# Kernel optimization log

Hardware: AMD Instinct MI355X
Metric: run time of the kernel (lower is better)

## Reference

```python
import jax, jax.numpy as jnp
from jax import lax
import numpy as np

B, T, F = 256, 256, 40
H, A, HORIZON = 256, 64, 60
D_SP = 192


def setup_inputs() -> dict:
    key = jax.random.key(0)
    ks = jax.random.split(key, 16)
    s = 0.05  # weight scale to keep activations stable
    return {
        'x': jax.random.normal(ks[0], (B, T, F), jnp.float32),
        'W_sp': jax.random.normal(ks[1], (F, D_SP), jnp.float32) * s,
        'b_sp': jnp.zeros((D_SP,), jnp.float32),
        'Wx_ef': jax.random.normal(ks[2], (D_SP, 4 * H), jnp.float32) * s,
        'Wh_ef': jax.random.normal(ks[3], (H, 4 * H), jnp.float32) * s,
        'b_ef': jnp.zeros((4 * H,), jnp.float32),
        'Wx_eb': jax.random.normal(ks[4], (D_SP, 4 * H), jnp.float32) * s,
        'Wh_eb': jax.random.normal(ks[5], (H, 4 * H), jnp.float32) * s,
        'b_eb': jnp.zeros((4 * H,), jnp.float32),
        'We': jax.random.normal(ks[6], (2 * H, A), jnp.float32) * s,
        'Wd': jax.random.normal(ks[7], (H, A), jnp.float32) * s,
        'v': jax.random.normal(ks[8], (A,), jnp.float32) * s,
        'Wx_d': jax.random.normal(ks[9], (1 + 2 * H, 4 * H), jnp.float32) * s,
        'Wh_d': jax.random.normal(ks[10], (H, 4 * H), jnp.float32) * s,
        'b_d': jnp.zeros((4 * H,), jnp.float32),
        'W_ih': jax.random.normal(ks[11], (2 * H, H), jnp.float32) * s,
        'b_ih': jnp.zeros((H,), jnp.float32),
        'W_ic': jax.random.normal(ks[12], (2 * H, H), jnp.float32) * s,
        'b_ic': jnp.zeros((H,), jnp.float32),
        'Wo': jax.random.normal(ks[13], (H, 1), jnp.float32) * s,
        'bo': jnp.zeros((1,), jnp.float32),
    }


def _lstm_cell(x_t, h, c, Wx, Wh, b):
    g = x_t @ Wx + h @ Wh + b
    i, f, gg, o = jnp.split(g, 4, axis=-1)  # torch gate order i,f,g,o
    c = jax.nn.sigmoid(f) * c + jax.nn.sigmoid(i) * jnp.tanh(gg)
    h = jax.nn.sigmoid(o) * jnp.tanh(c)
    return h, c


def _lstm_scan(xs_tbd, Wx, Wh, b):
    # xs_tbd: [T, B, D] -> hs [T, B, H]
    h0 = jnp.zeros((xs_tbd.shape[1], Wh.shape[0]), xs_tbd.dtype)
    c0 = jnp.zeros_like(h0)
    def step(carry, x_t):
        h, c = carry
        h, c = _lstm_cell(x_t, h, c, Wx, Wh, b)
        return (h, c), h
    _, hs = lax.scan(step, (h0, c0), xs_tbd)
    return hs


def reference(x, W_sp, b_sp, Wx_ef, Wh_ef, b_ef, Wx_eb, Wh_eb, b_eb,
              We, Wd, v, Wx_d, Wh_d, b_d, W_ih, b_ih, W_ic, b_ic, Wo, bo):
    # spatial encoder (stand-in for DeepLOBEncoder): [B,T,F] -> [B,T,192]
    h_spatial = x @ W_sp + b_sp
    xs = jnp.swapaxes(h_spatial, 0, 1)          # [T, B, 192]
    hs_f = _lstm_scan(xs, Wx_ef, Wh_ef, b_ef)    # [T, B, H]
    hs_b = _lstm_scan(xs[::-1], Wx_eb, Wh_eb, b_eb)[::-1]
    enc_out = jnp.swapaxes(jnp.concatenate([hs_f, hs_b], axis=-1), 0, 1)  # [B,T,2H]

    enc_mean = enc_out.mean(axis=1)
    dec_h = jnp.tanh(enc_mean @ W_ih + b_ih)     # [B, H]
    dec_c = jnp.tanh(enc_mean @ W_ic + b_ic)

    enc_proj = enc_out @ We                      # [B, T, A] precomputed (same math)
    prev_y = ((x[:, -1, 0] + x[:, -1, 2]) / 2.0)[:, None]  # ask_idx=0, bid_idx=2

    def dec_step(carry, _):
        h, c, py = carry
        e = jnp.tanh(enc_proj + (h @ Wd)[:, None, :])        # [B,T,A]
        scores = e @ v                                        # [B,T]
        w = jax.nn.softmax(scores, axis=1)
        context = jnp.einsum('bt,bth->bh', w, enc_out)        # [B,2H]
        dec_in = jnp.concatenate([py, context], axis=1)       # [B,1+2H]
        h, c = _lstm_cell(dec_in, h, c, Wx_d, Wh_d, b_d)
        y = h @ Wo + bo                                       # [B,1]
        return (h, c, lax.stop_gradient(y)), y[:, 0]

    _, ys = lax.scan(dec_step, (dec_h, dec_c, prev_y), None, length=HORIZON)
    return jnp.swapaxes(ys, 0, 1)  # [B, horizon]
```

## Files before the change

kernel.cpp:

```cpp
#include <hip/hip_runtime.h>
#include <cmath>

#define B_ 256
#define T_ 256
#define F_ 40
#define H_ 256
#define A_ 64
#define HOR_ 60
#define DSP_ 192
#define ENC_NBLK 128
#define GRP_SZ 16
#define WSTR 456

typedef unsigned short u16;
typedef unsigned int u32;
typedef __attribute__((ext_vector_type(8))) short bf16x8;
typedef __attribute__((ext_vector_type(4))) float f32x4;
typedef __attribute__((ext_vector_type(8))) u32 u32x8;
typedef __attribute__((ext_vector_type(4))) u32 u32x4;

__device__ __forceinline__ float sigm(float x){ return 1.f/(1.f+expf(-x)); }

__device__ __forceinline__ u16 f2bf(float x){
  u32 u = __float_as_uint(x);
  u32 r = (u + 0x7FFFu + ((u>>16)&1u)) >> 16;
  return (u16)r;
}
__device__ __forceinline__ float bf2f(u16 h){ return __uint_as_float(((u32)h)<<16); }
__device__ __forceinline__ u32 packsplit(float x){
  u16 hi = f2bf(x);
  u16 lo = f2bf(x - bf2f(hi));
  return (u32)hi | ((u32)lo<<16);
}
__device__ __forceinline__ float unpack2f(u32 v){
  return __uint_as_float(v<<16) + __uint_as_float(v & 0xFFFF0000u);
}

__device__ __forceinline__ float wred_sum(float v){
  #pragma unroll
  for (int o=32;o>0;o>>=1) v += __shfl_xor(v,o);
  return v;
}
__device__ __forceinline__ float wred_max(float v){
  #pragma unroll
  for (int o=32;o>0;o>>=1) v = fmaxf(v,__shfl_xor(v,o));
  return v;
}

__global__ void conv_w(const float* __restrict__ Wx, const float* __restrict__ Wh,
                       u16* __restrict__ hi, u16* __restrict__ lo,
                       int KX, int Ktot, int N){
  int idx = blockIdx.x*256 + threadIdx.x;
  if (idx >= N*Ktot) return;
  int n = idx / Ktot, k = idx - n*Ktot;
  float w = (k < KX) ? Wx[(size_t)k*N + n] : Wh[(size_t)(k-KX)*N + n];
  u16 h = f2bf(w);
  hi[idx] = h;
  lo[idx] = f2bf(w - bf2f(h));
}

__global__ __launch_bounds__(192) void spatial_proj(
    const float* __restrict__ x, const float* __restrict__ W, const float* __restrict__ bsp,
    u32* __restrict__ hsp32){
  __shared__ float Ws[40][192];
  __shared__ float xr[40];
  int t = blockIdx.x, tid = threadIdx.x;
  for (int i = tid; i < 40*192; i += 192){ int k = i/192, c = i-k*192; Ws[k][c] = W[i]; }
  float bb = bsp[tid];
  __syncthreads();
  for (int b=0; b<B_; b++){
    if (tid < 40) xr[tid] = x[((size_t)b*T_ + t)*F_ + tid];
    __syncthreads();
    float acc = bb;
    #pragma unroll
    for (int k=0;k<40;k++) acc += xr[k]*Ws[k][tid];
    hsp32[((size_t)t*B_ + b)*DSP_ + tid] = packsplit(acc);
    __syncthreads();
  }
}

__global__ __launch_bounds__(256) void enc_scan(
    const u32* __restrict__ hsp32,
    const u16* __restrict__ W_hi, const u16* __restrict__ W_lo,
    const float* __restrict__ b_ef, const float* __restrict__ b_eb,
    u32* __restrict__ hbuf, u32* __restrict__ eo32, int* __restrict__ bar)
{
  extern __shared__ u16 smem[];
  u16* Whi = smem;
  u16* Wlo = smem + 4*16*WSTR;
  const int bid = blockIdx.x;
  const int grp = bid & 7;
  const int nt  = bid >> 3;
  const int dir = grp >> 2;
  const int m0  = (grp & 3) * 64;
  const int u0  = nt * 16;
  const int tid = threadIdx.x;
  const int wave = tid >> 6, lane = tid & 63;
  const int lrow = lane & 15, kblk = lane >> 4;
  const int koff = kblk * 8;
  {
    const size_t wbase = ((size_t)dir*1024 + u0) * 448;
    for (int idx = tid; idx < 4*16*448; idx += 256){
      int g = idx / (16*448);
      int r = idx - g*(16*448);
      int j = r / 448;
      int k = r - j*448;
      size_t go = wbase + ((size_t)g*256 + j)*448 + k;
      Whi[(g*16 + j)*WSTR + k] = W_hi[go];
      Wlo[(g*16 + j)*WSTR + k] = W_lo[go];
    }
  }
  const float* bias = dir ? b_eb : b_ef;
  float bg4[4];
  #pragma unroll
  for (int g=0; g<4; g++) bg4[g] = bias[g*H_ + u0 + lrow];
  __syncthreads();

  const int mrow = m0 + wave*16;
  const int arow = mrow + lrow;
  u32* hP0 = hbuf + (size_t)dir*(B_*H_);
  u32* hP1 = hbuf + (size_t)(2+dir)*(B_*H_);
  int* gbar = bar + grp*T_;
  float c_reg[4] = {0.f,0.f,0.f,0.f};

  for (int s=0; s<T_; s++){
    const int t = dir ? (T_-1-s) : s;
    f32x4 acc[4] = {};
    const u32* abase = hsp32 + ((size_t)t*B_ + arow)*DSP_;
    #pragma unroll
    for (int ks=0; ks<6; ks++){
      int kb = ks*32 + koff;
      u32x8 la = *(const u32x8*)(abase + kb);
      bf16x8 ah, al;
      #pragma unroll
      for (int j=0;j<8;j++){ ah[j]=(short)(la[j]&0xFFFFu); al[j]=(short)(la[j]>>16); }
      #pragma unroll
      for (int g=0; g<4; g++){
        bf16x8 bh = *(const bf16x8*)(Whi + (g*16+lrow)*WSTR + kb);
        bf16x8 bl = *(const bf16x8*)(Wlo + (g*16+lrow)*WSTR + kb);
        acc[g] = __builtin_amdgcn_mfma_f32_16x16x32_bf16(ah, bh, acc[g], 0,0,0);
        acc[g] = __builtin_amdgcn_mfma_f32_16x16x32_bf16(ah, bl, acc[g], 0,0,0);
        acc[g] = __builtin_amdgcn_mfma_f32_16x16x32_bf16(al, bh, acc[g], 0,0,0);
      }
    }
    if (s > 0){
      if (tid == 0){
        while (__hip_atomic_load(&gbar[s-1], __ATOMIC_ACQUIRE, __HIP_MEMORY_SCOPE_AGENT) < GRP_SZ)
          __builtin_amdgcn_s_sleep(1);
      }
      __syncthreads();
    }
    const u32* hin = (s & 1) ? hP1 : hP0;
    u32* hout      = (s & 1) ? hP0 : hP1;
    const u32* hbase = hin + (size_t)arow*H_;
    #pragma unroll
    for (int ks=0; ks<8; ks++){
      int kb = ks*32 + koff;
      u32x8 la = *(const u32x8*)(hbase + kb);
      bf16x8 ah, al;
      #pragma unroll
      for (int j=0;j<8;j++){ ah[j]=(short)(la[j]&0xFFFFu); al[j]=(short)(la[j]>>16); }
      #pragma unroll
      for (int g=0; g<4; g++){
        bf16x8 bh = *(const bf16x8*)(Whi + (g*16+lrow)*WSTR + 192 + kb);
        bf16x8 bl = *(const bf16x8*)(Wlo + (g*16+lrow)*WSTR + 192 + kb);
        acc[g] = __builtin_amdgcn_mfma_f32_16x16x32_bf16(ah, bh, acc[g], 0,0,0);
        acc[g] = __builtin_amdgcn_mfma_f32_16x16x32_bf16(ah, bl, acc[g], 0,0,0);
        acc[g] = __builtin_amdgcn_mfma_f32_16x16x32_bf16(al, bh, acc[g], 0,0,0);
      }
    }
    #pragma unroll
    for (int r=0; r<4; r++){
      int brow = mrow + kblk*4 + r;
      float gi = acc[0][r] + bg4[0];
      float gf = acc[1][r] + bg4[1];
      float gg = acc[2][r] + bg4[2];
      float go = acc[3][r] + bg4[3];
      float cn = sigm(gf)*c_reg[r] + sigm(gi)*tanhf(gg);
      float hn = sigm(go)*tanhf(cn);
      c_reg[r] = cn;
      u32 hp = packsplit(hn);
      hout[(size_t)brow*H_ + u0 + lrow] = hp;
      __builtin_nontemporal_store(hp, &eo32[((size_t)brow*T_ + t)*512 + dir*H_ + u0 + lrow]);
    }
    if (s == T_-1) break;
    __syncthreads();
    if (tid == 0)
      __hip_atomic_fetch_add(&gbar[s], 1, __ATOMIC_RELEASE, __HIP_MEMORY_SCOPE_AGENT);
  }
}

__global__ __launch_bounds__(128) void dec_step_mfma(
    const u32* __restrict__ Ad32,
    const u16* __restrict__ W_hi, const u16* __restrict__ W_lo,
    const float* __restrict__ b_d, const float* __restrict__ Wx_d,
    const float* __restrict__ py,
    float* __restrict__ c_dec, float* __restrict__ h_dec,
    u32* __restrict__ AdW)
{
  const int u0 = blockIdx.x * 16;
  const int tid = threadIdx.x;
  const int wave = tid >> 6, lane = tid & 63;
  const int lrow = lane & 15, kblk = lane >> 4;
  const int u = u0 + lrow;
  const int mbase = blockIdx.y * 32 + wave * 16;
  const int koff = kblk * 8;
  size_t wro[4];
  #pragma unroll
  for (int g=0; g<4; g++) wro[g] = (size_t)(g*H_ + u) * 768;
  f32x4 acc[4] = {};
  const u32* abase = Ad32 + (size_t)(mbase + lrow)*768;
  for (int ks=0; ks<24; ks++){
    int kb = ks*32 + koff;
    u32x8 ld = *(const u32x8*)(abase + kb);
    bf16x8 ah, al;
    #pragma unroll
    for (int j=0;j<8;j++){ ah[j] = (short)(ld[j] & 0xFFFFu); al[j] = (short)(ld[j] >> 16); }
    #pragma unroll
    for (int g=0; g<4; g++){
      bf16x8 bh = *(const bf16x8*)(W_hi + wro[g] + kb);
      bf16x8 bl = *(const bf16x8*)(W_lo + wro[g] + kb);
      acc[g] = __builtin_amdgcn_mfma_f32_16x16x32_bf16(ah, bh, acc[g], 0,0,0);
      acc[g] = __builtin_amdgcn_mfma_f32_16x16x32_bf16(ah, bl, acc[g], 0,0,0);
      acc[g] = __builtin_amdgcn_mfma_f32_16x16x32_bf16(al, bh, acc[g], 0,0,0);
    }
  }
  float bg4[4], w0g[4];
  #pragma unroll
  for (int g=0;g<4;g++){ bg4[g] = b_d[g*H_ + u]; w0g[g] = Wx_d[g*H_ + u]; }
  #pragma unroll
  for (int r=0; r<4; r++){
    int b = mbase + kblk*4 + r;
    float pyb = py[b];
    float gi = acc[0][r] + bg4[0] + pyb*w0g[0];
    float gf = acc[1][r] + bg4[1] + pyb*w0g[1];
    float gg = acc[2][r] + bg4[2] + pyb*w0g[2];
    float go = acc[3][r] + bg4[3] + pyb*w0g[3];
    size_t ci = (size_t)b*H_ + u;
    float cn = sigm(gf)*c_dec[ci] + sigm(gi)*tanhf(gg);
    float hn = sigm(go)*tanhf(cn);
    c_dec[ci] = cn;
    h_dec[ci] = hn;
    AdW[(size_t)b*768 + 512 + u] = packsplit(hn);
  }
}

__global__ __launch_bounds__(256) void gemm_ep(
    const u32* __restrict__ eo32, const u16* __restrict__ Wet_hi, const u16* __restrict__ Wet_lo,
    float* __restrict__ ep)
{
  const int tid = threadIdx.x, wave = tid>>6, lane = tid&63;
  const int lrow = lane&15, kblk = lane>>4, koff = kblk*8;
  const size_t arow = (size_t)blockIdx.x*64 + wave*16 + lrow;
  f32x4 acc[4] = {};
  size_t wro[4];
  #pragma unroll
  for (int nf=0; nf<4; nf++) wro[nf] = (size_t)(nf*16 + lrow)*512;
  for (int ks=0; ks<16; ks++){
    int kb = ks*32 + koff;
    u32x8 ld = *(const u32x8*)(eo32 + arow*512 + kb);
    bf16x8 ah, al;
    #pragma unroll
    for (int j=0;j<8;j++){ ah[j] = (short)(ld[j] & 0xFFFFu); al[j] = (short)(ld[j] >> 16); }
    #pragma unroll
    for (int nf=0; nf<4; nf++){
      bf16x8 bh = *(const bf16x8*)(Wet_hi + wro[nf] + kb);
      bf16x8 bl = *(const bf16x8*)(Wet_lo + wro[nf] + kb);
      acc[nf] = __builtin_amdgcn_mfma_f32_16x16x32_bf16(ah, bh, acc[nf], 0,0,0);
      acc[nf] = __builtin_amdgcn_mfma_f32_16x16x32_bf16(ah, bl, acc[nf], 0,0,0);
      acc[nf] = __builtin_amdgcn_mfma_f32_16x16x32_bf16(al, bh, acc[nf], 0,0,0);
    }
  }
  #pragma unroll
  for (int nf=0; nf<4; nf++)
    #pragma unroll
    for (int r=0; r<4; r++){
      size_t orow = (size_t)blockIdx.x*64 + wave*16 + kblk*4 + r;
      ep[orow*64 + nf*16 + lrow] = acc[nf][r];
    }
}

__global__ __launch_bounds__(256) void sgemm_bias(
    const float* __restrict__ A, const float* __restrict__ W,
    const float* __restrict__ bias, float* __restrict__ C,
    int M, int N, int K, int act)
{
  __shared__ float As[64][17];
  __shared__ float Ws[16][64];
  int tid = threadIdx.x;
  int tr = tid >> 4, tc = tid & 15;
  int row0 = blockIdx.y * 64, col0 = blockIdx.x * 64;
  float acc[4][4] = {};
  for (int k0 = 0; k0 < K; k0 += 16) {
    for (int i = tid; i < 64*16; i += 256) {
      int r = i >> 4, kk = i & 15;
      int gr = row0 + r, gk = k0 + kk;
      As[r][kk] = (gr < M && gk < K) ? A[(size_t)gr*K + gk] : 0.f;
    }
    for (int i = tid; i < 16*64; i += 256) {
      int r = i >> 6, c = i & 63;
      int gk = k0 + r, gc = col0 + c;
      Ws[r][c] = (gk < K && gc < N) ? W[(size_t)gk*N + gc] : 0.f;
    }
    __syncthreads();
    #pragma unroll
    for (int kk=0;kk<16;kk++){
      float a0 = As[tr*4+0][kk], a1 = As[tr*4+1][kk];
      float a2v = As[tr*4+2][kk], a3 = As[tr*4+3][kk];
      float4 b4 = *(const float4*)&Ws[kk][tc*4];
      acc[0][0]+=a0*b4.x; acc[0][1]+=a0*b4.y; acc[0][2]+=a0*b4.z; acc[0][3]+=a0*b4.w;
      acc[1][0]+=a1*b4.x; acc[1][1]+=a1*b4.y; acc[1][2]+=a1*b4.z; acc[1][3]+=a1*b4.w;
      acc[2][0]+=a2v*b4.x; acc[2][1]+=a2v*b4.y; acc[2][2]+=a2v*b4.z; acc[2][3]+=a2v*b4.w;
      acc[3][0]+=a3*b4.x; acc[3][1]+=a3*b4.y; acc[3][2]+=a3*b4.z; acc[3][3]+=a3*b4.w;
    }
    __syncthreads();
  }
  #pragma unroll
  for (int i=0;i<4;i++){
    int r = row0 + tr*4 + i; if (r >= M) continue;
    #pragma unroll
    for (int j=0;j<4;j++){
      int c = col0 + tc*4 + j; if (c >= N) continue;
      float vv = acc[i][j] + (bias ? bias[c] : 0.f);
      if (act == 1) vv = tanhf(vv);
      C[(size_t)r*N + c] = vv;
    }
  }
}

__global__ __launch_bounds__(256) void attn_step(
    const u32* __restrict__ eo32, const float* __restrict__ ep,
    const float* __restrict__ Wd, const float* __restrict__ v,
    const float* __restrict__ Wo, const float* __restrict__ bo,
    const float* __restrict__ h_dec, u32* __restrict__ Ad32,
    float* __restrict__ py, float* __restrict__ out, int s)
{
  __shared__ float sh_h[256], sh_hwd[64], sh_v[64], sh_sc[256], sh_w[256];
  __shared__ float red4[4][64];
  __shared__ float sh_red[4], sh_red2[4];
  __shared__ float redc[4][512];
  int b = blockIdx.x, tid = threadIdx.x;
  int wave = tid >> 6, lane = tid & 63;
  float hv = h_dec[b*H_ + tid];
  sh_h[tid] = hv;
  if (tid < 64) sh_v[tid] = v[tid];
  __syncthreads();
  if (s > 0) {
    float p = hv * Wo[tid];
    p = wred_sum(p);
    if ((tid & 63) == 0) sh_red[tid>>6] = p;
    __syncthreads();
    if (tid == 0) {
      float y = sh_red[0]+sh_red[1]+sh_red[2]+sh_red[3] + bo[0];
      out[b*HOR_ + (s-1)] = y;
      py[b] = y;
    }
  }
  {
    int a = tid & 63, q = tid >> 6;
    float ssum = 0.f;
    for (int j=q*64; j<q*64+64; j++) ssum += sh_h[j]*Wd[(size_t)j*A_ + a];
    red4[q][a] = ssum;
    __syncthreads();
    if (tid < 64) sh_hwd[tid] = red4[0][tid]+red4[1][tid]+red4[2][tid]+red4[3][tid];
  }
  __syncthreads();
  int aa = tid & 3;
  #pragma unroll
  for (int p=0;p<4;p++){
    int t = p*64 + (tid>>2);
    const float4* ep4 = (const float4*)(ep + ((size_t)(b*T_+t))*A_ + aa*16);
    float partial = 0.f;
    #pragma unroll
    for (int q=0;q<4;q++){
      float4 e4 = ep4[q];
      int a0 = aa*16 + q*4;
      partial += tanhf(e4.x + sh_hwd[a0+0]) * sh_v[a0+0];
      partial += tanhf(e4.y + sh_hwd[a0+1]) * sh_v[a0+1];
      partial += tanhf(e4.z + sh_hwd[a0+2]) * sh_v[a0+2];
      partial += tanhf(e4.w + sh_hwd[a0+3]) * sh_v[a0+3];
    }
    partial += __shfl_xor(partial, 1);
    partial += __shfl_xor(partial, 2);
    if (aa == 0) sh_sc[t] = partial;
  }
  __syncthreads();
  float sc = sh_sc[tid];
  float m = wred_max(sc);
  if ((tid&63)==0) sh_red[tid>>6] = m;
  __syncthreads();
  m = fmaxf(fmaxf(sh_red[0],sh_red[1]), fmaxf(sh_red[2],sh_red[3]));
  float e = expf(sc - m);
  float su = wred_sum(e);
  if ((tid&63)==0) sh_red2[tid>>6] = su;
  __syncthreads();
  su = (sh_red2[0]+sh_red2[1])+(sh_red2[2]+sh_red2[3]);
  sh_w[tid] = e / su;
  __syncthreads();
  float cacc[8] = {};
  const u32* eo = eo32 + (size_t)b*T_*512 + lane*8;
  #pragma unroll 4
  for (int tt=0; tt<64; tt++){
    int t = wave*64 + tt;
    float wgt = sh_w[t];
    u32x4 e0 = *(const u32x4*)(eo + (size_t)t*512);
    u32x4 e1 = *(const u32x4*)(eo + (size_t)t*512 + 4);
    #pragma unroll
    for (int j=0;j<4;j++){
      cacc[j]   += wgt * unpack2f(e0[j]);
      cacc[4+j] += wgt * unpack2f(e1[j]);
    }
  }
  #pragma unroll
  for (int j=0;j<8;j++) redc[wave][lane*8+j] = cacc[j];
  __syncthreads();
  float c0 = redc[0][tid]+redc[1][tid]+redc[2][tid]+redc[3][tid];
  float c1 = redc[0][256+tid]+redc[1][256+tid]+redc[2][256+tid]+redc[3][256+tid];
  Ad32[(size_t)b*768 + tid]       = packsplit(c0);
  Ad32[(size_t)b*768 + 256 + tid] = packsplit(c1);
}

__global__ __launch_bounds__(256) void final_y(const float* __restrict__ h_dec,
    const float* __restrict__ Wo, const float* __restrict__ bo, float* __restrict__ out){
  __shared__ float sh[4];
  int b = blockIdx.x, tid = threadIdx.x;
  float p = h_dec[b*H_+tid]*Wo[tid];
  p = wred_sum(p);
  if ((tid&63)==0) sh[tid>>6]=p;
  __syncthreads();
  if (tid==0) out[b*HOR_ + HOR_-1] = sh[0]+sh[1]+sh[2]+sh[3] + bo[0];
}

__global__ __launch_bounds__(256) void enc_mean_k(const u32* __restrict__ eo32,
                                                  float* __restrict__ em){
  __shared__ float redc[4][512];
  int b = blockIdx.x, tid = threadIdx.x;
  int wave = tid >> 6, lane = tid & 63;
  float cacc[8] = {};
  const u32* eo = eo32 + (size_t)b*T_*512 + lane*8;
  #pragma unroll 4
  for (int tt=0; tt<64; tt++){
    int t = wave*64 + tt;
    u32x4 e0 = *(const u32x4*)(eo + (size_t)t*512);
    u32x4 e1 = *(const u32x4*)(eo + (size_t)t*512 + 4);
    #pragma unroll
    for (int j=0;j<4;j++){ cacc[j] += unpack2f(e0[j]); cacc[4+j] += unpack2f(e1[j]); }
  }
  #pragma unroll
  for (int j=0;j<8;j++) redc[wave][lane*8+j] = cacc[j];
  __syncthreads();
  em[(size_t)b*512 + tid]       = (redc[0][tid]+redc[1][tid]+redc[2][tid]+redc[3][tid])*(1.f/T_);
  em[(size_t)b*512 + 256 + tid] = (redc[0][256+tid]+redc[1][256+tid]+redc[2][256+tid]+redc[3][256+tid])*(1.f/T_);
}

__global__ void pack_hd(const float* __restrict__ hd, u32* __restrict__ Ad32){
  int i = blockIdx.x*256 + threadIdx.x;
  int b = i >> 8, u = i & 255;
  Ad32[(size_t)b*768 + 512 + u] = packsplit(hd[i]);
}

__global__ void py_init(const float* __restrict__ x, float* __restrict__ py){
  int b = blockIdx.x*256 + threadIdx.x;
  if (b < B_)
    py[b] = (x[(size_t)b*T_*F_ + 255*F_ + 0] +
             x[(size_t)b*T_*F_ + 255*F_ + 2]) * 0.5f;
}

extern "C" void kernel_launch(void* const* d_in, const int* in_sizes, int n_in,
                              void* d_out, int out_size, void* d_ws, size_t ws_size,
                              hipStream_t stream)
{
  const float* x    = (const float*)d_in[0];
  const float* W_sp = (const float*)d_in[1];
  const float* b_sp = (const float*)d_in[2];
  const float* Wx_ef= (const float*)d_in[3];
  const float* Wh_ef= (const float*)d_in[4];
  const float* b_ef = (const float*)d_in[5];
  const float* Wx_eb= (const float*)d_in[6];
  const float* Wh_eb= (const float*)d_in[7];
  const float* b_eb = (const float*)d_in[8];
  const float* We   = (const float*)d_in[9];
  const float* Wd   = (const float*)d_in[10];
  const float* v    = (const float*)d_in[11];
  const float* Wx_d = (const float*)d_in[12];
  const float* Wh_d = (const float*)d_in[13];
  const float* b_d  = (const float*)d_in[14];
  const float* W_ih = (const float*)d_in[15];
  const float* b_ih = (const float*)d_in[16];
  const float* W_ic = (const float*)d_in[17];
  const float* b_ic = (const float*)d_in[18];
  const float* Wo   = (const float*)d_in[19];
  const float* bo   = (const float*)d_in[20];
  float* out = (float*)d_out;

  char* base = (char*)d_ws;
  auto alloc = [&](size_t bytes)->char*{
    char* p = base; base += (bytes + 255) & ~(size_t)255; return p;
  };
  u16* Wenc_hi = (u16*)alloc((size_t)2*1024*448*2);
  u16* Wenc_lo = (u16*)alloc((size_t)2*1024*448*2);
  u16* Wdec_hi = (u16*)alloc((size_t)1024*768*2);
  u16* Wdec_lo = (u16*)alloc((size_t)1024*768*2);
  u16* Wet_hi  = (u16*)alloc((size_t)64*512*2);
  u16* Wet_lo  = (u16*)alloc((size_t)64*512*2);
  u32* hsp32   = (u32*)alloc((size_t)T_*B_*DSP_*4);
  u32* hbuf    = (u32*)alloc((size_t)2*2*B_*H_*4);
  u32* eo32    = (u32*)alloc((size_t)B_*T_*512*4);
  float* em    = (float*)alloc((size_t)B_*512*4);
  float* ep    = (float*)alloc((size_t)B_*T_*64*4);
  float* hd    = (float*)alloc((size_t)B_*H_*4);
  float* cd    = (float*)alloc((size_t)B_*H_*4);
  u32* Ad32    = (u32*)alloc((size_t)B_*768*4);
  float* pyb   = (float*)alloc((size_t)B_*4);
  int* bar     = (int*)alloc((size_t)8*T_*4);
  if ((size_t)(base - (char*)d_ws) > ws_size) return;

  conv_w<<<dim3(1792),256,0,stream>>>(Wx_ef, Wh_ef, Wenc_hi, Wenc_lo, DSP_, 448, 1024);
  conv_w<<<dim3(1792),256,0,stream>>>(Wx_eb, Wh_eb, Wenc_hi+458752, Wenc_lo+458752, DSP_, 448, 1024);
  conv_w<<<dim3(3072),256,0,stream>>>(Wx_d+1024, Wh_d, Wdec_hi, Wdec_lo, 512, 768, 1024);
  conv_w<<<dim3(128),256,0,stream>>>(We, We, Wet_hi, Wet_lo, 512, 512, 64);

  spatial_proj<<<dim3(256),192,0,stream>>>(x, W_sp, b_sp, hsp32);

  hipMemsetAsync(hbuf, 0, (size_t)2*B_*H_*4, stream);
  hipMemsetAsync(bar, 0, (size_t)8*T_*4, stream);

  enc_scan<<<dim3(ENC_NBLK), dim3(256), 2*4*16*WSTR*2, stream>>>(
      hsp32, Wenc_hi, Wenc_lo, b_ef, b_eb, hbuf, eo32, bar);

  enc_mean_k<<<dim3(256),256,0,stream>>>(eo32, em);
  sgemm_bias<<<dim3(4,4),256,0,stream>>>(em, W_ih, b_ih, hd, B_, H_, 2*H_, 1);
  sgemm_bias<<<dim3(4,4),256,0,stream>>>(em, W_ic, b_ic, cd, B_, H_, 2*H_, 1);
  pack_hd<<<dim3(256),256,0,stream>>>(hd, Ad32);
  gemm_ep<<<dim3(1024),256,0,stream>>>(eo32, Wet_hi, Wet_lo, ep);
  py_init<<<dim3(1),256,0,stream>>>(x, pyb);

  for (int s=0; s<HOR_; s++){
    attn_step<<<dim3(256),256,0,stream>>>(eo32, ep, Wd, v, Wo, bo, hd, Ad32, pyb, out, s);
    dec_step_mfma<<<dim3(16,8),128,0,stream>>>(Ad32, Wdec_hi, Wdec_lo, b_d, Wx_d, pyb, cd, hd, Ad32);
  }
  final_y<<<dim3(256),256,0,stream>>>(hd, Wo, bo, out);
}
```

Before: 6.543 ms.

## Fuse decoder attention and LSTM steps into one persistent kernel over batch rows

```diff
diff --git a/kernel.cpp b/kernel.cpp
--- a/kernel.cpp
+++ b/kernel.cpp
@@ -190,58 +190,159 @@
   }
 }
 
-__global__ __launch_bounds__(128) void dec_step_mfma(
-    const u32* __restrict__ Ad32,
+__global__ __launch_bounds__(256) void dec_all(
+    const u32* __restrict__ eo32, const float* __restrict__ ep,
+    const float* __restrict__ Wd, const float* __restrict__ v,
+    const float* __restrict__ Wo, const float* __restrict__ bo,
     const u16* __restrict__ W_hi, const u16* __restrict__ W_lo,
     const float* __restrict__ b_d, const float* __restrict__ Wx_d,
-    const float* __restrict__ py,
-    float* __restrict__ c_dec, float* __restrict__ h_dec,
-    u32* __restrict__ AdW)
+    const float* __restrict__ hd0, const float* __restrict__ cd0,
+    const float* __restrict__ x, float* __restrict__ out)
 {
-  const int u0 = blockIdx.x * 16;
+  __shared__ __align__(32) u32 din[4][768];
+  __shared__ float hfp[4][256];
+  __shared__ float cst[4][256];
+  __shared__ float wsm[4][256];
+  __shared__ float hwd[4][64];
+  __shared__ float py4[4];
+  __shared__ float bgl[1024], w0l[1024];
+  const int row0 = blockIdx.x*4;
   const int tid = threadIdx.x;
-  const int wave = tid >> 6, lane = tid & 63;
-  const int lrow = lane & 15, kblk = lane >> 4;
-  const int u = u0 + lrow;
-  const int mbase = blockIdx.y * 32 + wave * 16;
-  const int koff = kblk * 8;
-  size_t wro[4];
-  #pragma unroll
-  for (int g=0; g<4; g++) wro[g] = (size_t)(g*H_ + u) * 768;
-  f32x4 acc[4] = {};
-  const u32* abase = Ad32 + (size_t)(mbase + lrow)*768;
-  for (int ks=0; ks<24; ks++){
-    int kb = ks*32 + koff;
-    u32x8 ld = *(const u32x8*)(abase + kb);
-    bf16x8 ah, al;
-    #pragma unroll
-    for (int j=0;j<8;j++){ ah[j] = (short)(ld[j] & 0xFFFFu); al[j] = (short)(ld[j] >> 16); }
-    #pragma unroll
-    for (int g=0; g<4; g++){
-      bf16x8 bh = *(const bf16x8*)(W_hi + wro[g] + kb);
-      bf16x8 bl = *(const bf16x8*)(W_lo + wro[g] + kb);
-      acc[g] = __builtin_amdgcn_mfma_f32_16x16x32_bf16(ah, bh, acc[g], 0,0,0);
-      acc[g] = __builtin_amdgcn_mfma_f32_16x16x32_bf16(ah, bl, acc[g], 0,0,0);
-      acc[g] = __builtin_amdgcn_mfma_f32_16x16x32_bf16(al, bh, acc[g], 0,0,0);
-    }
-  }
-  float bg4[4], w0g[4];
-  #pragma unroll
-  for (int g=0;g<4;g++){ bg4[g] = b_d[g*H_ + u]; w0g[g] = Wx_d[g*H_ + u]; }
-  #pragma unroll
-  for (int r=0; r<4; r++){
-    int b = mbase + kblk*4 + r;
-    float pyb = py[b];
-    float gi = acc[0][r] + bg4[0] + pyb*w0g[0];
-    float gf = acc[1][r] + bg4[1] + pyb*w0g[1];
-    float gg = acc[2][r] + bg4[2] + pyb*w0g[2];
-    float go = acc[3][r] + bg4[3] + pyb*w0g[3];
-    size_t ci = (size_t)b*H_ + u;
-    float cn = sigm(gf)*c_dec[ci] + sigm(gi)*tanhf(gg);
-    float hn = sigm(go)*tanhf(cn);
-    c_dec[ci] = cn;
-    h_dec[ci] = hn;
-    AdW[(size_t)b*768 + 512 + u] = packsplit(hn);
+  const int wave = tid>>6, lane = tid&63;
+
+  #pragma unroll
+  for (int r=0;r<4;r++){
+    float h0 = hd0[(size_t)(row0+r)*H_ + tid];
+    hfp[r][tid] = h0;
+    cst[r][tid] = cd0[(size_t)(row0+r)*H_ + tid];
+    din[r][512+tid] = packsplit(h0);
+  }
+  #pragma unroll
+  for (int i=0;i<4;i++){
+    bgl[tid+i*256] = b_d[tid+i*256];
+    w0l[tid+i*256] = Wx_d[tid+i*256];
+  }
+  if (tid < 4){
+    size_t xb = ((size_t)(row0+tid)*T_ + 255)*F_;
+    py4[tid] = (x[xb] + x[xb+2])*0.5f;
+  }
+  __syncthreads();
+
+  for (int s=0; s<=HOR_; s++){
+    if (s > 0){
+      float p = hfp[wave][lane]*Wo[lane] + hfp[wave][lane+64]*Wo[lane+64]
+              + hfp[wave][lane+128]*Wo[lane+128] + hfp[wave][lane+192]*Wo[lane+192];
+      p = wred_sum(p);
+      if (lane == 0){
+        float y = p + bo[0];
+        out[(size_t)(row0+wave)*HOR_ + (s-1)] = y;
+        py4[wave] = y;
+      }
+      __syncthreads();
+    }
+    if (s == HOR_) break;
+    {
+      float a = 0.f;
+      for (int j=0;j<H_;j++) a += hfp[wave][j]*Wd[(size_t)j*A_ + lane];
+      hwd[wave][lane] = a;
+    }
+    __syncthreads();
+    {
+      const int t = tid;
+      #pragma unroll
+      for (int r=0;r<4;r++){
+        const float4* ep4 = (const float4*)(ep + ((size_t)(row0+r)*T_ + t)*A_);
+        float sc = 0.f;
+        #pragma unroll
+        for (int q=0;q<16;q++){
+          float4 e4 = ep4[q];
+          int a0 = q*4;
+          sc += tanhf(e4.x+hwd[r][a0+0])*v[a0+0];
+          sc += tanhf(e4.y+hwd[r][a0+1])*v[a0+1];
+          sc += tanhf(e4.z+hwd[r][a0+2])*v[a0+2];
+          sc += tanhf(e4.w+hwd[r][a0+3])*v[a0+3];
+        }
+        wsm[r][t] = sc;
+      }
+    }
+    __syncthreads();
+    {
+      const int r = wave;
+      float s0=wsm[r][lane], s1=wsm[r][lane+64], s2=wsm[r][lane+128], s3=wsm[r][lane+192];
+      float mx = wred_max(fmaxf(fmaxf(s0,s1),fmaxf(s2,s3)));
+      float e0=expf(s0-mx), e1=expf(s1-mx), e2=expf(s2-mx), e3=expf(s3-mx);
+      float inv = 1.f / wred_sum((e0+e1)+(e2+e3));
+      wsm[r][lane]=e0*inv; wsm[r][lane+64]=e1*inv; wsm[r][lane+128]=e2*inv; wsm[r][lane+192]=e3*inv;
+    }
+    {
+      const int r = wave;
+      float cacc[8] = {0.f,0.f,0.f,0.f,0.f,0.f,0.f,0.f};
+      const u32* eo = eo32 + (size_t)(row0+r)*T_*512 + lane*8;
+      #pragma unroll 4
+      for (int t=0;t<T_;t++){
+        float wgt = wsm[r][t];
+        u32x4 e0 = *(const u32x4*)(eo + (size_t)t*512);
+        u32x4 e1 = *(const u32x4*)(eo + (size_t)t*512 + 4);
+        #pragma unroll
+        for (int j=0;j<4;j++){
+          cacc[j]   += wgt*unpack2f(e0[j]);
+          cacc[4+j] += wgt*unpack2f(e1[j]);
+        }
+      }
+      #pragma unroll
+      for (int j=0;j<8;j++) din[r][lane*8+j] = packsplit(cacc[j]);
+    }
+    __syncthreads();
+    {
+      const int r4 = lane & 15;
+      const int kblk = lane >> 4, koff = kblk*8;
+      f32x4 acc[4][4] = {};
+      for (int ks=0; ks<24; ks++){
+        int kb = ks*32 + koff;
+        bf16x8 ah, al;
+        if (r4 < 4){
+          u32x8 ld = *(const u32x8*)(&din[r4][kb]);
+          #pragma unroll
+          for (int j=0;j<8;j++){ ah[j]=(short)(ld[j]&0xFFFFu); al[j]=(short)(ld[j]>>16); }
+        } else {
+          #pragma unroll
+          for (int j=0;j<8;j++){ ah[j]=0; al[j]=0; }
+        }
+        #pragma unroll
+        for (int ut=0; ut<4; ut++){
+          #pragma unroll
+          for (int g=0; g<4; g++){
+            size_t n = (size_t)(g*256 + wave*64 + ut*16 + r4)*768;
+            bf16x8 bh = *(const bf16x8*)(W_hi + n + kb);
+            bf16x8 bl = *(const bf16x8*)(W_lo + n + kb);
+            acc[ut][g] = __builtin_amdgcn_mfma_f32_16x16x32_bf16(ah, bh, acc[ut][g], 0,0,0);
+            acc[ut][g] = __builtin_amdgcn_mfma_f32_16x16x32_bf16(ah, bl, acc[ut][g], 0,0,0);
+            acc[ut][g] = __builtin_amdgcn_mfma_f32_16x16x32_bf16(al, bh, acc[ut][g], 0,0,0);
+          }
+        }
+      }
+      __syncthreads();
+      if (kblk == 0){
+        #pragma unroll
+        for (int ut=0; ut<4; ut++){
+          int u = wave*64 + ut*16 + r4;
+          #pragma unroll
+          for (int r=0;r<4;r++){
+            float pyr = py4[r];
+            float gi = acc[ut][0][r] + bgl[u]     + pyr*w0l[u];
+            float gf = acc[ut][1][r] + bgl[256+u] + pyr*w0l[256+u];
+            float gg = acc[ut][2][r] + bgl[512+u] + pyr*w0l[512+u];
+            float go = acc[ut][3][r] + bgl[768+u] + pyr*w0l[768+u];
+            float cn = sigm(gf)*cst[r][u] + sigm(gi)*tanhf(gg);
+            float hn = sigm(go)*tanhf(cn);
+            cst[r][u] = cn;
+            hfp[r][u] = hn;
+            din[r][512+u] = packsplit(hn);
+          }
+        }
+      }
+    }
+    __syncthreads();
   }
 }
 
@@ -328,109 +429,6 @@
   }
 }
 
-__global__ __launch_bounds__(256) void attn_step(
-    const u32* __restrict__ eo32, const float* __restrict__ ep,
-    const float* __restrict__ Wd, const float* __restrict__ v,
-    const float* __restrict__ Wo, const float* __restrict__ bo,
-    const float* __restrict__ h_dec, u32* __restrict__ Ad32,
-    float* __restrict__ py, float* __restrict__ out, int s)
-{
-  __shared__ float sh_h[256], sh_hwd[64], sh_v[64], sh_sc[256], sh_w[256];
-  __shared__ float red4[4][64];
-  __shared__ float sh_red[4], sh_red2[4];
-  __shared__ float redc[4][512];
-  int b = blockIdx.x, tid = threadIdx.x;
-  int wave = tid >> 6, lane = tid & 63;
-  float hv = h_dec[b*H_ + tid];
-  sh_h[tid] = hv;
-  if (tid < 64) sh_v[tid] = v[tid];
-  __syncthreads();
-  if (s > 0) {
-    float p = hv * Wo[tid];
-    p = wred_sum(p);
-    if ((tid & 63) == 0) sh_red[tid>>6] = p;
-    __syncthreads();
-    if (tid == 0) {
-      float y = sh_red[0]+sh_red[1]+sh_red[2]+sh_red[3] + bo[0];
-      out[b*HOR_ + (s-1)] = y;
-      py[b] = y;
-    }
-  }
-  {
-    int a = tid & 63, q = tid >> 6;
-    float ssum = 0.f;
-    for (int j=q*64; j<q*64+64; j++) ssum += sh_h[j]*Wd[(size_t)j*A_ + a];
-    red4[q][a] = ssum;
-    __syncthreads();
-    if (tid < 64) sh_hwd[tid] = red4[0][tid]+red4[1][tid]+red4[2][tid]+red4[3][tid];
-  }
-  __syncthreads();
-  int aa = tid & 3;
-  #pragma unroll
-  for (int p=0;p<4;p++){
-    int t = p*64 + (tid>>2);
-    const float4* ep4 = (const float4*)(ep + ((size_t)(b*T_+t))*A_ + aa*16);
-    float partial = 0.f;
-    #pragma unroll
-    for (int q=0;q<4;q++){
-      float4 e4 = ep4[q];
-      int a0 = aa*16 + q*4;
-      partial += tanhf(e4.x + sh_hwd[a0+0]) * sh_v[a0+0];
-      partial += tanhf(e4.y + sh_hwd[a0+1]) * sh_v[a0+1];
-      partial += tanhf(e4.z + sh_hwd[a0+2]) * sh_v[a0+2];
-      partial += tanhf(e4.w + sh_hwd[a0+3]) * sh_v[a0+3];
-    }
-    partial += __shfl_xor(partial, 1);
-    partial += __shfl_xor(partial, 2);
-    if (aa == 0) sh_sc[t] = partial;
-  }
-  __syncthreads();
-  float sc = sh_sc[tid];
-  float m = wred_max(sc);
-  if ((tid&63)==0) sh_red[tid>>6] = m;
-  __syncthreads();
-  m = fmaxf(fmaxf(sh_red[0],sh_red[1]), fmaxf(sh_red[2],sh_red[3]));
-  float e = expf(sc - m);
-  float su = wred_sum(e);
-  if ((tid&63)==0) sh_red2[tid>>6] = su;
-  __syncthreads();
-  su = (sh_red2[0]+sh_red2[1])+(sh_red2[2]+sh_red2[3]);
-  sh_w[tid] = e / su;
-  __syncthreads();
-  float cacc[8] = {};
-  const u32* eo = eo32 + (size_t)b*T_*512 + lane*8;
-  #pragma unroll 4
-  for (int tt=0; tt<64; tt++){
-    int t = wave*64 + tt;
-    float wgt = sh_w[t];
-    u32x4 e0 = *(const u32x4*)(eo + (size_t)t*512);
-    u32x4 e1 = *(const u32x4*)(eo + (size_t)t*512 + 4);
-    #pragma unroll
-    for (int j=0;j<4;j++){
-      cacc[j]   += wgt * unpack2f(e0[j]);
-      cacc[4+j] += wgt * unpack2f(e1[j]);
-    }
-  }
-  #pragma unroll
-  for (int j=0;j<8;j++) redc[wave][lane*8+j] = cacc[j];
-  __syncthreads();
-  float c0 = redc[0][tid]+redc[1][tid]+redc[2][tid]+redc[3][tid];
-  float c1 = redc[0][256+tid]+redc[1][256+tid]+redc[2][256+tid]+redc[3][256+tid];
-  Ad32[(size_t)b*768 + tid]       = packsplit(c0);
-  Ad32[(size_t)b*768 + 256 + tid] = packsplit(c1);
-}
-
-__global__ __launch_bounds__(256) void final_y(const float* __restrict__ h_dec,
-    const float* __restrict__ Wo, const float* __restrict__ bo, float* __restrict__ out){
-  __shared__ float sh[4];
-  int b = blockIdx.x, tid = threadIdx.x;
-  float p = h_dec[b*H_+tid]*Wo[tid];
-  p = wred_sum(p);
-  if ((tid&63)==0) sh[tid>>6]=p;
-  __syncthreads();
-  if (tid==0) out[b*HOR_ + HOR_-1] = sh[0]+sh[1]+sh[2]+sh[3] + bo[0];
-}
-
 __global__ __launch_bounds__(256) void enc_mean_k(const u32* __restrict__ eo32,
                                                   float* __restrict__ em){
   __shared__ float redc[4][512];
@@ -438,7 +436,7 @@
   int wave = tid >> 6, lane = tid & 63;
   float cacc[8] = {};
   const u32* eo = eo32 + (size_t)b*T_*512 + lane*8;
-  #pragma unroll 4
+  #pragma unroll 8
   for (int tt=0; tt<64; tt++){
     int t = wave*64 + tt;
     u32x4 e0 = *(const u32x4*)(eo + (size_t)t*512);
@@ -451,19 +449,6 @@
   __syncthreads();
   em[(size_t)b*512 + tid]       = (redc[0][tid]+redc[1][tid]+redc[2][tid]+redc[3][tid])*(1.f/T_);
   em[(size_t)b*512 + 256 + tid] = (redc[0][256+tid]+redc[1][256+tid]+redc[2][256+tid]+redc[3][256+tid])*(1.f/T_);
-}
-
-__global__ void pack_hd(const float* __restrict__ hd, u32* __restrict__ Ad32){
-  int i = blockIdx.x*256 + threadIdx.x;
-  int b = i >> 8, u = i & 255;
-  Ad32[(size_t)b*768 + 512 + u] = packsplit(hd[i]);
-}
-
-__global__ void py_init(const float* __restrict__ x, float* __restrict__ py){
-  int b = blockIdx.x*256 + threadIdx.x;
-  if (b < B_)
-    py[b] = (x[(size_t)b*T_*F_ + 255*F_ + 0] +
-             x[(size_t)b*T_*F_ + 255*F_ + 2]) * 0.5f;
 }
 
 extern "C" void kernel_launch(void* const* d_in, const int* in_sizes, int n_in,
@@ -510,8 +495,6 @@
   float* ep    = (float*)alloc((size_t)B_*T_*64*4);
   float* hd    = (float*)alloc((size_t)B_*H_*4);
   float* cd    = (float*)alloc((size_t)B_*H_*4);
-  u32* Ad32    = (u32*)alloc((size_t)B_*768*4);
-  float* pyb   = (float*)alloc((size_t)B_*4);
   int* bar     = (int*)alloc((size_t)8*T_*4);
   if ((size_t)(base - (char*)d_ws) > ws_size) return;
 
@@ -531,13 +514,8 @@
   enc_mean_k<<<dim3(256),256,0,stream>>>(eo32, em);
   sgemm_bias<<<dim3(4,4),256,0,stream>>>(em, W_ih, b_ih, hd, B_, H_, 2*H_, 1);
   sgemm_bias<<<dim3(4,4),256,0,stream>>>(em, W_ic, b_ic, cd, B_, H_, 2*H_, 1);
-  pack_hd<<<dim3(256),256,0,stream>>>(hd, Ad32);
   gemm_ep<<<dim3(1024),256,0,stream>>>(eo32, Wet_hi, Wet_lo, ep);
-  py_init<<<dim3(1),256,0,stream>>>(x, pyb);
-
-  for (int s=0; s<HOR_; s++){
-    attn_step<<<dim3(256),256,0,stream>>>(eo32, ep, Wd, v, Wo, bo, hd, Ad32, pyb, out, s);
-    dec_step_mfma<<<dim3(16,8),128,0,stream>>>(Ad32, Wdec_hi, Wdec_lo, b_d, Wx_d, pyb, cd, hd, Ad32);
-  }
-  final_y<<<dim3(256),256,0,stream>>>(hd, Wo, bo, out);
-}
+
+  dec_all<<<dim3(64),256,0,stream>>>(
+      eo32, ep, Wd, v, Wo, bo, Wdec_hi, Wdec_lo, b_d, Wx_d, hd, cd, x, out);
+}
```

Result: slower. 12.07 ms (+84.5%).
